# Optimization experiments

Hardware: AMD Instinct MI355X
Metric: run time of the kernel (lower is better)

## Reference

```python
import jax, jax.numpy as jnp
import numpy as np

K = 3  # kernel_size

def _hamming2d(k):
    h = np.hamming(k)
    return (np.outer(h, h)).astype(np.float32)

def setup_inputs() -> dict:
    key = jax.random.key(0)
    k1, k2 = jax.random.split(key)
    x = jax.random.normal(k1, (8, 64, 128, 128), dtype=jnp.float32)
    W = jax.random.normal(k2, (9, 64, 3, 3), dtype=jnp.float32) * 0.001
    b = jnp.zeros((9,), dtype=jnp.float32)
    return {"x": x, "W": W, "b": b}

def reference(x, W, b):
    B, C, H, Wd = x.shape
    # filter generator: 3x3 conv, padding=1 -> (B, K*K, H, W)
    mask = jax.lax.conv_general_dilated(
        x, W, window_strides=(1, 1), padding=((1, 1), (1, 1)),
        dimension_numbers=("NCHW", "OIHW", "NCHW")) + b[None, :, None, None]
    # kernel normalizer: softmax over the K*K taps, hamming reweight, renormalize
    mask = jax.nn.softmax(mask, axis=1)
    ham = jnp.asarray(_hamming2d(K).reshape(-1))  # (K*K,)
    mask = mask * ham[None, :, None, None]
    mask = mask / jnp.sum(mask, axis=1, keepdims=True)
    # carafe (up=1): weighted sum of KxK shifted neighborhoods, reflect-padded.
    pad = K // 2
    xp = jnp.pad(x, ((0, 0), (0, 0), (pad, pad), (pad, pad)), mode="reflect")
    lowpass = jnp.zeros_like(x)
    for idx in range(K * K):
        i, j = divmod(idx, K)
        lowpass = lowpass + xp[:, :, i:i + H, j:j + Wd] * mask[:, idx:idx + 1]
    # highpass = x - lowpass; residual output = x + highpass
    return 2.0 * x - lowpass
```

## Files before the change

kernel.cpp:

```cpp
#include <hip/hip_runtime.h>


typedef __attribute__((ext_vector_type(8))) short short8;
typedef __attribute__((ext_vector_type(4))) float floatx4;
typedef __attribute__((ext_vector_type(4))) unsigned uint4v;
typedef __attribute__((ext_vector_type(2))) float float2v;

#define IH 128
#define IW 128
#define CCH 64
#define TSX 16
#define TSY 8
#define TPX 18
#define TPY 10
#define CSH 72

__device__ __forceinline__ unsigned short f2bf(float f) {
    unsigned u = __float_as_uint(f);
    u += 0x7FFFu + ((u >> 16) & 1u);
    return (unsigned short)(u >> 16);
}
__device__ __forceinline__ unsigned cvtpk(float a, float b) {
    unsigned r;
    asm("v_cvt_pk_bf16_f32 %0, %1, %2" : "=v"(r) : "v"(a), "v"(b));
    return r;
}
__device__ __forceinline__ float2v unpk(unsigned u) {
    float2v r;
    r.x = __uint_as_float(u << 16);
    r.y = __uint_as_float(u & 0xFFFF0000u);
    return r;
}

__global__ void ahpf_prep(const float* __restrict__ Wg,
                          unsigned short* __restrict__ wsp)
{
    const int i = blockIdx.x * 256 + threadIdx.x;
    if (i >= 18 * 64) return;
    const int s = i >> 6, l = i & 63;
    const int fm = l & 15, fq = l >> 4;
    const int tap = s >> 1, cb = (s & 1) * 32 + fq * 8;
    short8 v = (short8)0;
    if (fm < 9) {
#pragma unroll
        for (int jj = 0; jj < 8; ++jj)
            v[jj] = (short)f2bf(Wg[fm * 576 + (cb + jj) * 9 + tap]);
    }
    ((short8*)wsp)[i] = v;
}

template <bool USE_WS>
__global__ __launch_bounds__(128, 2) void ahpf_kernel(
    const float* __restrict__ x, const float* __restrict__ Wg,
    const float* __restrict__ bias, float* __restrict__ out,
    const unsigned short* __restrict__ wsp)
{
    __shared__ __align__(16) unsigned short sx[TPY * TPX * CSH];

    const int tid  = threadIdx.x;
    const int lane = tid & 63;
    const int wv   = tid >> 6;

    const unsigned flat = blockIdx.x + 8u * (blockIdx.y + 16u * blockIdx.z);
    const unsigned nid  = (flat & 7u) * 128u + (flat >> 3);
    const int bx = nid & 7, by = (nid >> 3) & 15, bz = nid >> 7;

    const int ty0 = by * TSY;
    const int tx0 = bx * TSX;
    const size_t hw = (size_t)IH * IW;
    const float* xb = x + (size_t)bz * CCH * hw;

    const int fm = lane & 15;
    const int fq = lane >> 4;

    short8 afr[18];
    if (USE_WS) {
        const short8* wf = (const short8*)wsp;
#pragma unroll
        for (int s = 0; s < 18; ++s) afr[s] = wf[s * 64 + lane];
    } else {
#pragma unroll
        for (int s = 0; s < 18; ++s) {
            short8 a = (short8)0;
            if (fm < 9) {
                const int tap = s >> 1, cb = (s & 1) * 32 + fq * 8;
                const float* wp = Wg + fm * 576 + tap;
#pragma unroll
                for (int jj = 0; jj < 8; ++jj)
                    a[jj] = (short)f2bf(wp[(cb + jj) * 9]);
            }
            afr[s] = a;
        }
    }
    float bq[4];
#pragma unroll
    for (int r = 0; r < 4; ++r) {
        const int t = fq * 4 + r;
        bq[r] = (t < 9) ? bias[t] : 0.0f;
    }

    {
        int gx0 = tx0 - 4;
        if (gx0 < 0) gx0 = 0;
        if (gx0 > IW - 24) gx0 = IW - 24;
        const bool xlo = (bx == 0), xhi = (bx == 7);
        const int cg8 = tid & 7;
#pragma unroll
        for (int it = 0; it < 4; ++it) {
            const int s = it * 128 + tid;
            if (s >= 480) break;
            const int u = s >> 3;
            const int y = u / 6, xg = u - 6 * y;
            int gy = ty0 + y - 1;
            gy = gy < 0 ? -gy : (gy >= IH ? 2 * IH - 2 - gy : gy);
            const float* src = xb + (size_t)(cg8 * 8) * hw
                             + (size_t)gy * IW + gx0 + 4 * xg;
            float4 v[8];
#pragma unroll
            for (int jj = 0; jj < 8; ++jj)
                v[jj] = *(const float4*)(src + (size_t)jj * hw);
            const int xbase = gx0 + 4 * xg - tx0 + 1;
#pragma unroll
            for (int e = 0; e < 4; ++e) {
                const float fe[8] = {
                    ((const float*)&v[0])[e], ((const float*)&v[1])[e],
                    ((const float*)&v[2])[e], ((const float*)&v[3])[e],
                    ((const float*)&v[4])[e], ((const float*)&v[5])[e],
                    ((const float*)&v[6])[e], ((const float*)&v[7])[e]};
                uint4v pk;
                pk.x = cvtpk(fe[0], fe[1]); pk.y = cvtpk(fe[2], fe[3]);
                pk.z = cvtpk(fe[4], fe[5]); pk.w = cvtpk(fe[6], fe[7]);
                const int gxe = gx0 + 4 * xg + e;
                const int xx = xbase + e;
                if (xx >= 0 && xx < TPX)
                    *(uint4v*)&sx[(y * TPX + xx) * CSH + cg8 * 8] = pk;
                if (xlo && gxe == 1)
                    *(uint4v*)&sx[(y * TPX + 0) * CSH + cg8 * 8] = pk;
                if (xhi && gxe == 126)
                    *(uint4v*)&sx[(y * TPX + 17) * CSH + cg8 * 8] = pk;
            }
        }
    }
    __syncthreads();

    const bool border = (bx == 0) | (bx == 7) | (by == 0) | (by == 15);
    const int n = fm;

    for (int rr = 0; rr < 4; ++rr) {
        const int R = wv * 4 + rr;
        const int h = ty0 + R, w = tx0 + n;

        short8 bfr[18];
#pragma unroll
        for (int s = 0; s < 18; ++s) {
            const int tap = s >> 1;
            const int dy = tap / 3 - 1, dx = tap % 3 - 1;
            bfr[s] = *(const short8*)&sx[((R + 1 + dy) * TPX + (n + 1 + dx)) * CSH
                                         + (s & 1) * 32 + fq * 8];
        }

        floatx4 acc = {0.f, 0.f, 0.f, 0.f};
        if (border) {
#pragma unroll
            for (int s = 0; s < 18; ++s) {
                const int tap = s >> 1;
                const int dy = tap / 3 - 1, dx = tap % 3 - 1;
                const int hy = h + dy, wx = w + dx;
                short8 bb = bfr[s];
                if (hy < 0 || hy >= IH || wx < 0 || wx >= IW) bb = (short8)0;
                acc = __builtin_amdgcn_mfma_f32_16x16x32_bf16(afr[s], bb, acc, 0, 0, 0);
            }
        } else {
#pragma unroll
            for (int s = 0; s < 18; ++s)
                acc = __builtin_amdgcn_mfma_f32_16x16x32_bf16(afr[s], bfr[s], acc, 0, 0, 0);
        }

        auto hamt = [](int t) {
            const float a = (t / 3 == 1) ? 1.f : 0.08f;
            const float b = (t % 3 == 1) ? 1.f : 0.08f;
            return a * b;
        };
        const int nval = (fq < 2) ? 4 : (fq == 2 ? 1 : 0);
        float e0 = 0, e1 = 0, e2 = 0, e3 = 0, ssum = 0;
        if (nval >= 1) { e0 = __expf(acc[0] + bq[0]) * hamt(fq * 4 + 0); ssum += e0; }
        if (nval >= 4) { e1 = __expf(acc[1] + bq[1]) * hamt(fq * 4 + 1); ssum += e1;
                         e2 = __expf(acc[2] + bq[2]) * hamt(fq * 4 + 2); ssum += e2;
                         e3 = __expf(acc[3] + bq[3]) * hamt(fq * 4 + 3); ssum += e3; }
        ssum += __shfl_xor(ssum, 16);
        ssum += __shfl_xor(ssum, 32);
        const float inv = 1.0f / ssum;

        const unsigned p01 = cvtpk(e0 * inv, e1 * inv);
        const unsigned p23 = cvtpk(e2 * inv, e3 * inv);
        const unsigned q0 = (unsigned)__shfl((int)p01, n);
        const unsigned q1 = (unsigned)__shfl((int)p23, n);
        const unsigned q2 = (unsigned)__shfl((int)p01, 16 + n);
        const unsigned q3 = (unsigned)__shfl((int)p23, 16 + n);
        const unsigned q4 = (unsigned)__shfl((int)p01, 32 + n);
        float mk[9];
        { float2v m;
          m = unpk(q0); mk[0] = m.x; mk[1] = m.y;
          m = unpk(q1); mk[2] = m.x; mk[3] = m.y;
          m = unpk(q2); mk[4] = m.x; mk[5] = m.y;
          m = unpk(q3); mk[6] = m.x; mk[7] = m.y;
          mk[8] = unpk(q4).x; }

        float2v l[8];
#pragma unroll
        for (int q = 0; q < 8; ++q) l[q] = (float2v)0.f;
#pragma unroll
        for (int t = 0; t < 9; ++t) {
            const float mt = mk[t];
            const uint4v b0 = *(const uint4v*)&bfr[2 * t];
            const uint4v b1 = *(const uint4v*)&bfr[2 * t + 1];
#pragma unroll
            for (int q = 0; q < 4; ++q) {
                l[q]     += mt * unpk(b0[q]);
                l[q + 4] += mt * unpk(b1[q]);
            }
        }
        const uint4v c0 = *(const uint4v*)&bfr[8];
        const uint4v c1 = *(const uint4v*)&bfr[9];
        float* ob = out + (size_t)bz * CCH * hw + (size_t)h * IW + w
                  + (size_t)(8 * fq) * hw;
#pragma unroll
        for (int q = 0; q < 4; ++q) {
            const float2v oe = 2.f * unpk(c0[q]) - l[q];
            const float2v oo = 2.f * unpk(c1[q]) - l[q + 4];
            ob[(size_t)(2 * q) * hw]          = oe.x;
            ob[(size_t)(2 * q + 1) * hw]      = oe.y;
            ob[(size_t)(32 + 2 * q) * hw]     = oo.x;
            ob[(size_t)(32 + 2 * q + 1) * hw] = oo.y;
        }
    }
}

extern "C" void kernel_launch(void* const* d_in, const int* in_sizes, int n_in,
                              void* d_out, int out_size, void* d_ws, size_t ws_size,
                              hipStream_t stream) {
    const float* x    = (const float*)d_in[0];
    const float* Wg   = (const float*)d_in[1];
    const float* bias = (const float*)d_in[2];
    float* out        = (float*)d_out;
    const int B = in_sizes[0] / (CCH * IH * IW);
    dim3 grid(8, 16, B);

    if (ws_size >= 18 * 64 * 16) {
        unsigned short* wsp = (unsigned short*)d_ws;
        ahpf_prep<<<5, 256, 0, stream>>>(Wg, wsp);
        ahpf_kernel<true><<<grid, dim3(128, 1, 1), 0, stream>>>(x, Wg, bias, out, wsp);
    } else {
        ahpf_kernel<false><<<grid, dim3(128, 1, 1), 0, stream>>>(x, Wg, bias, out, nullptr);
    }
}
```

Before: 100.1 us.

## Reuse shared-memory neighborhood rows across output rows and use bf16 dot2 for CARAFE

Each wave processes four consecutive output rows. Instead of reloading all 18 shared-memory fragments for every row, it now shifts the 12 fragments that overlap the previous row and loads only the 6 for the new bottom row, which cuts LDS reads. The per-tap weighted sum used to unpack bf16 to fp32 and do scalar FMAs. It now pairs two taps with v_perm_b32 and accumulates them with v_dot2_f32_bf16, roughly halving the ALU instructions for that step. The cost is higher register pressure, since bfr now lives across the fully unrolled row loop, plus some extra permute instructions.

```diff
diff --git a/kernel.cpp b/kernel.cpp
--- a/kernel.cpp
+++ b/kernel.cpp
@@ -15,6 +15,9 @@
 #define TPY 10
 #define CSH 72
 
+#define SELLO 0x05040100u
+#define SELHI 0x07060302u
+
 __device__ __forceinline__ unsigned short f2bf(float f) {
     unsigned u = __float_as_uint(f);
     u += 0x7FFFu + ((u >> 16) & 1u);
@@ -30,6 +33,15 @@
     r.x = __uint_as_float(u << 16);
     r.y = __uint_as_float(u & 0xFFFF0000u);
     return r;
+}
+__device__ __forceinline__ unsigned permb(unsigned hi, unsigned lo, unsigned sel) {
+    unsigned d;
+    asm("v_perm_b32 %0, %1, %2, %3" : "=v"(d) : "v"(hi), "v"(lo), "s"(sel));
+    return d;
+}
+__device__ __forceinline__ float dot2bf(unsigned x2, unsigned m2, float acc) {
+    asm("v_dot2_f32_bf16 %0, %1, %2, %0" : "+v"(acc) : "v"(x2), "v"(m2));
+    return acc;
 }
 
 __global__ void ahpf_prep(const float* __restrict__ Wg,
@@ -146,17 +158,44 @@
     const bool border = (bx == 0) | (bx == 7) | (by == 0) | (by == 15);
     const int n = fm;
 
+#define CARAFE_PAIR(sa, sb, qq)                                              \
+    {                                                                        \
+        const uint4v A0 = *(const uint4v*)&bfr[(sa)];                        \
+        const uint4v B0 = *(const uint4v*)&bfr[(sb)];                        \
+        const uint4v A1 = *(const uint4v*)&bfr[(sa) + 1];                    \
+        const uint4v B1 = *(const uint4v*)&bfr[(sb) + 1];                    \
+        _Pragma("unroll")                                                    \
+        for (int u = 0; u < 4; ++u) {                                        \
+            l[2*u]       = dot2bf(permb(B0[u], A0[u], SELLO), qq, l[2*u]);   \
+            l[2*u + 1]   = dot2bf(permb(B0[u], A0[u], SELHI), qq, l[2*u+1]); \
+            l[8 + 2*u]   = dot2bf(permb(B1[u], A1[u], SELLO), qq, l[8+2*u]); \
+            l[8 + 2*u+1] = dot2bf(permb(B1[u], A1[u], SELHI), qq, l[8+2*u+1]);\
+        }                                                                    \
+    }
+
+    short8 bfr[18];
+#pragma unroll
     for (int rr = 0; rr < 4; ++rr) {
         const int R = wv * 4 + rr;
         const int h = ty0 + R, w = tx0 + n;
 
-        short8 bfr[18];
-#pragma unroll
-        for (int s = 0; s < 18; ++s) {
-            const int tap = s >> 1;
-            const int dy = tap / 3 - 1, dx = tap % 3 - 1;
-            bfr[s] = *(const short8*)&sx[((R + 1 + dy) * TPX + (n + 1 + dx)) * CSH
-                                         + (s & 1) * 32 + fq * 8];
+        if (rr == 0) {
+#pragma unroll
+            for (int s = 0; s < 18; ++s) {
+                const int tap = s >> 1;
+                const int dy = tap / 3 - 1, dx = tap % 3 - 1;
+                bfr[s] = *(const short8*)&sx[((R + 1 + dy) * TPX + (n + 1 + dx)) * CSH
+                                             + (s & 1) * 32 + fq * 8];
+            }
+        } else {
+#pragma unroll
+            for (int s = 0; s < 12; ++s) bfr[s] = bfr[s + 6];
+#pragma unroll
+            for (int s = 12; s < 18; ++s) {
+                const int dx = (s >> 1) % 3 - 1;
+                bfr[s] = *(const short8*)&sx[((R + 2) * TPX + (n + 1 + dx)) * CSH
+                                             + (s & 1) * 32 + fq * 8];
+            }
         }
 
         floatx4 acc = {0.f, 0.f, 0.f, 0.f};
@@ -198,42 +237,31 @@
         const unsigned q2 = (unsigned)__shfl((int)p01, 16 + n);
         const unsigned q3 = (unsigned)__shfl((int)p23, 16 + n);
         const unsigned q4 = (unsigned)__shfl((int)p01, 32 + n);
-        float mk[9];
-        { float2v m;
-          m = unpk(q0); mk[0] = m.x; mk[1] = m.y;
-          m = unpk(q1); mk[2] = m.x; mk[3] = m.y;
-          m = unpk(q2); mk[4] = m.x; mk[5] = m.y;
-          m = unpk(q3); mk[6] = m.x; mk[7] = m.y;
-          mk[8] = unpk(q4).x; }
-
-        float2v l[8];
-#pragma unroll
-        for (int q = 0; q < 8; ++q) l[q] = (float2v)0.f;
-#pragma unroll
-        for (int t = 0; t < 9; ++t) {
-            const float mt = mk[t];
-            const uint4v b0 = *(const uint4v*)&bfr[2 * t];
-            const uint4v b1 = *(const uint4v*)&bfr[2 * t + 1];
-#pragma unroll
-            for (int q = 0; q < 4; ++q) {
-                l[q]     += mt * unpk(b0[q]);
-                l[q + 4] += mt * unpk(b1[q]);
-            }
-        }
+
+        float l[16];
+#pragma unroll
+        for (int i = 0; i < 16; ++i) l[i] = 0.f;
+        CARAFE_PAIR(0,  2,  q0);
+        CARAFE_PAIR(4,  6,  q1);
+        CARAFE_PAIR(8,  10, q2);
+        CARAFE_PAIR(12, 14, q3);
+        CARAFE_PAIR(16, 16, q4);
+
         const uint4v c0 = *(const uint4v*)&bfr[8];
         const uint4v c1 = *(const uint4v*)&bfr[9];
         float* ob = out + (size_t)bz * CCH * hw + (size_t)h * IW + w
                   + (size_t)(8 * fq) * hw;
 #pragma unroll
         for (int q = 0; q < 4; ++q) {
-            const float2v oe = 2.f * unpk(c0[q]) - l[q];
-            const float2v oo = 2.f * unpk(c1[q]) - l[q + 4];
-            ob[(size_t)(2 * q) * hw]          = oe.x;
-            ob[(size_t)(2 * q + 1) * hw]      = oe.y;
-            ob[(size_t)(32 + 2 * q) * hw]     = oo.x;
-            ob[(size_t)(32 + 2 * q + 1) * hw] = oo.y;
-        }
-    }
+            const float2v ce = unpk(c0[q]);
+            const float2v co = unpk(c1[q]);
+            ob[(size_t)(2 * q) * hw]          = 2.f * ce.x - l[2 * q];
+            ob[(size_t)(2 * q + 1) * hw]      = 2.f * ce.y - l[2 * q + 1];
+            ob[(size_t)(32 + 2 * q) * hw]     = 2.f * co.x - l[8 + 2 * q];
+            ob[(size_t)(32 + 2 * q + 1) * hw] = 2.f * co.y - l[8 + 2 * q + 1];
+        }
+    }
+#undef CARAFE_PAIR
 }
 
 extern "C" void kernel_launch(void* const* d_in, const int* in_sizes, int n_in,
```

Measured after the change: 99.30 us. About the same (-0.8%).
